# Optimization experiments

Measured on AMD Instinct MI355X. Metric: run time of the kernel, lower is better.

The kernel has to match this reference:

```python
import jax, jax.numpy as jnp
import numpy as np

M, IN, OUT = 32, 4096, 16384

def setup_inputs() -> dict:
    key = jax.random.key(0)
    k1, k2, k3 = jax.random.split(key, 3)
    x = jax.random.normal(k1, (M, IN), dtype=jnp.float32)
    weight_q = jax.random.randint(k2, (OUT, IN), 0, 256, dtype=jnp.int32)  # uint8 codes
    bias = jax.random.normal(k3, (OUT,), dtype=jnp.float32)
    return {"x": x, "weight_q": weight_q, "zero": 128, "scale": jnp.float32(0.01), "bias": bias}

def reference(x, weight_q, zero, scale, bias):
    # Dequantize: w = scale * (q - zero), per-tensor affine
    w = scale * (weight_q.astype(jnp.float32) - jnp.float32(zero))  # [OUT, IN]
    # F.linear: y = x @ w.T + b
    return jnp.einsum('mi,oi->mo', x, w) + bias
```

## Files before the change

kernel.cpp:

```cpp
#include <hip/hip_runtime.h>

#define M_DIM 32
#define K_DIM 4096
#define N_DIM 16384

using short8 = __attribute__((ext_vector_type(8))) short;
using f32x4  = __attribute__((ext_vector_type(4))) float;

__device__ __forceinline__ ushort f2bf_rne(float f) {
    unsigned u = __float_as_uint(f);
    u += 0x7fffu + ((u >> 16) & 1u);
    return (ushort)(u >> 16);
}

__device__ __forceinline__ ushort i2bf_exact(int v) {
    return (ushort)(__float_as_uint((float)v) >> 16);
}

__global__ __launch_bounds__(256) void prep_x_kernel(const float* __restrict__ x,
                                                     ushort* __restrict__ xb) {
    int i = blockIdx.x * blockDim.x + threadIdx.x;
    float4 v = reinterpret_cast<const float4*>(x)[i];
    ushort4 o;
    o.x = f2bf_rne(v.x); o.y = f2bf_rne(v.y); o.z = f2bf_rne(v.z); o.w = f2bf_rne(v.w);
    reinterpret_cast<ushort4*>(xb)[i] = o;
}

__global__ __launch_bounds__(256, 4) void qgemm_kernel(
        const ushort* __restrict__ xb, const int* __restrict__ wq,
        const int* __restrict__ zerop, const float* __restrict__ scalep,
        const float* __restrict__ bias, float* __restrict__ out) {
    const int n0   = blockIdx.x << 4;
    const int wave = threadIdx.x >> 6;
    const int lane = threadIdx.x & 63;
    const int quad = lane >> 4;
    const int l16  = lane & 15;
    const int zero = *zerop;

    const int k0 = wave << 10;

    const ushort* ap0 = xb + (size_t)l16 * K_DIM + k0 + (quad << 3);
    const ushort* ap1 = ap0 + 16 * K_DIM;
    const int* bp = wq + (size_t)(n0 + l16) * K_DIM + k0 + (quad << 3);

    f32x4 acc0 = {0.f, 0.f, 0.f, 0.f};
    f32x4 acc1 = {0.f, 0.f, 0.f, 0.f};

    #pragma unroll 4
    for (int ks = 0; ks < 32; ++ks) {
        short8 a0 = *reinterpret_cast<const short8*>(ap0);
        short8 a1 = *reinterpret_cast<const short8*>(ap1);
        int4 b0 = *reinterpret_cast<const int4*>(bp);
        int4 b1 = *reinterpret_cast<const int4*>(bp + 4);

        short8 bf;
        bf[0] = (short)i2bf_exact(b0.x - zero);
        bf[1] = (short)i2bf_exact(b0.y - zero);
        bf[2] = (short)i2bf_exact(b0.z - zero);
        bf[3] = (short)i2bf_exact(b0.w - zero);
        bf[4] = (short)i2bf_exact(b1.x - zero);
        bf[5] = (short)i2bf_exact(b1.y - zero);
        bf[6] = (short)i2bf_exact(b1.z - zero);
        bf[7] = (short)i2bf_exact(b1.w - zero);

        acc0 = __builtin_amdgcn_mfma_f32_16x16x32_bf16(a0, bf, acc0, 0, 0, 0);
        acc1 = __builtin_amdgcn_mfma_f32_16x16x32_bf16(a1, bf, acc1, 0, 0, 0);

        ap0 += 32; ap1 += 32; bp += 32;
    }

    __shared__ float red[4][32][16];
    #pragma unroll
    for (int i = 0; i < 4; ++i) {
        red[wave][(quad << 2) + i][l16]      = acc0[i];
        red[wave][16 + (quad << 2) + i][l16] = acc1[i];
    }
    __syncthreads();

    const float scale = *scalep;
    #pragma unroll
    for (int t = 0; t < 2; ++t) {
        int idx = threadIdx.x + (t << 8);
        int row = idx >> 4;
        int c   = idx & 15;
        float s = red[0][row][c] + red[1][row][c] + red[2][row][c] + red[3][row][c];
        out[(size_t)row * N_DIM + n0 + c] = fmaf(scale, s, bias[n0 + c]);
    }
}

extern "C" void kernel_launch(void* const* d_in, const int* in_sizes, int n_in,
                              void* d_out, int out_size, void* d_ws, size_t ws_size,
                              hipStream_t stream) {
    const float* x      = (const float*)d_in[0];
    const int*   wq     = (const int*)d_in[1];
    const int*   zerop  = (const int*)d_in[2];
    const float* scalep = (const float*)d_in[3];
    const float* bias   = (const float*)d_in[4];
    float*       out    = (float*)d_out;
    ushort*      xb     = (ushort*)d_ws;

    prep_x_kernel<<<(M_DIM * K_DIM / 4) / 256, 256, 0, stream>>>(x, xb);
    qgemm_kernel<<<N_DIM / 16, 256, 0, stream>>>(xb, wq, zerop, scalep, bias, out);
}
```

Measured before the change: 376.5 us.

## Stage weight tiles through LDS with coalesced loads, register prefetch and staggered K order

Weight loads now go through a shared-memory tile. Each wave reads contiguous 128-element K chunks of its rows (coalesced int4 loads), converts them to bf16 into LDS, and the MFMA operands are read back from LDS. The next chunk is prefetched into registers while the current one is consumed. Each block starts at a different K phase, which spreads accesses across memory channels. In exchange it adds two __syncthreads per stage and drops the occupancy hint from launch bounds.

```diff
diff --git a/kernel.cpp b/kernel.cpp
--- a/kernel.cpp
+++ b/kernel.cpp
@@ -3,6 +3,10 @@
 #define M_DIM 32
 #define K_DIM 4096
 #define N_DIM 16384
+#define BN 16
+#define BK 128
+#define NSTAGE 32
+#define LROW 136
 
 using short8 = __attribute__((ext_vector_type(8))) short;
 using f32x4  = __attribute__((ext_vector_type(4))) float;
@@ -17,6 +21,15 @@
     return (ushort)(__float_as_uint((float)v) >> 16);
 }
 
+__device__ __forceinline__ ushort4 cvt4(int4 v, int zero) {
+    ushort4 o;
+    o.x = i2bf_exact(v.x - zero);
+    o.y = i2bf_exact(v.y - zero);
+    o.z = i2bf_exact(v.z - zero);
+    o.w = i2bf_exact(v.w - zero);
+    return o;
+}
+
 __global__ __launch_bounds__(256) void prep_x_kernel(const float* __restrict__ x,
                                                      ushort* __restrict__ xb) {
     int i = blockIdx.x * blockDim.x + threadIdx.x;
@@ -26,50 +39,62 @@
     reinterpret_cast<ushort4*>(xb)[i] = o;
 }
 
-__global__ __launch_bounds__(256, 4) void qgemm_kernel(
+__global__ __launch_bounds__(256) void qgemm_kernel(
         const ushort* __restrict__ xb, const int* __restrict__ wq,
         const int* __restrict__ zerop, const float* __restrict__ scalep,
         const float* __restrict__ bias, float* __restrict__ out) {
-    const int n0   = blockIdx.x << 4;
-    const int wave = threadIdx.x >> 6;
-    const int lane = threadIdx.x & 63;
+    __shared__ ushort tile[BN][LROW];
+    __shared__ float  red[4][M_DIM][BN];
+
+    const int tid  = threadIdx.x;
+    const int wave = tid >> 6;
+    const int lane = tid & 63;
     const int quad = lane >> 4;
     const int l16  = lane & 15;
+    const int n0   = blockIdx.x * BN;
     const int zero = *zerop;
+    const int phase = blockIdx.x & (NSTAGE - 1);
 
-    const int k0 = wave << 10;
+    const int srow0 = wave * 4 + (lane >> 5);
+    const int srow1 = srow0 + 2;
+    const int sofs  = (lane & 31) * 4;
+    const int* gb0 = wq + (size_t)(n0 + srow0) * K_DIM + sofs;
+    const int* gb1 = wq + (size_t)(n0 + srow1) * K_DIM + sofs;
 
-    const ushort* ap0 = xb + (size_t)l16 * K_DIM + k0 + (quad << 3);
-    const ushort* ap1 = ap0 + 16 * K_DIM;
-    const int* bp = wq + (size_t)(n0 + l16) * K_DIM + k0 + (quad << 3);
+    const int bofs = wave * 32 + quad * 8;
+    const ushort* axp0 = xb + (size_t)l16 * K_DIM + bofs;
+    const ushort* axp1 = axp0 + 16 * K_DIM;
 
     f32x4 acc0 = {0.f, 0.f, 0.f, 0.f};
     f32x4 acc1 = {0.f, 0.f, 0.f, 0.f};
 
-    #pragma unroll 4
-    for (int ks = 0; ks < 32; ++ks) {
-        short8 a0 = *reinterpret_cast<const short8*>(ap0);
-        short8 a1 = *reinterpret_cast<const short8*>(ap1);
-        int4 b0 = *reinterpret_cast<const int4*>(bp);
-        int4 b1 = *reinterpret_cast<const int4*>(bp + 4);
+    int4 c0 = *(const int4*)(gb0 + phase * BK);
+    int4 c1 = *(const int4*)(gb1 + phase * BK);
 
-        short8 bf;
-        bf[0] = (short)i2bf_exact(b0.x - zero);
-        bf[1] = (short)i2bf_exact(b0.y - zero);
-        bf[2] = (short)i2bf_exact(b0.z - zero);
-        bf[3] = (short)i2bf_exact(b0.w - zero);
-        bf[4] = (short)i2bf_exact(b1.x - zero);
-        bf[5] = (short)i2bf_exact(b1.y - zero);
-        bf[6] = (short)i2bf_exact(b1.z - zero);
-        bf[7] = (short)i2bf_exact(b1.w - zero);
+    #pragma unroll 1
+    for (int s = 0; s < NSTAGE; ++s) {
+        int4 nx0, nx1;
+        if (s + 1 < NSTAGE) {
+            int sn = ((s + 1 + phase) & (NSTAGE - 1)) * BK;
+            nx0 = *(const int4*)(gb0 + sn);
+            nx1 = *(const int4*)(gb1 + sn);
+        }
+        __syncthreads();
+        *(ushort4*)&tile[srow0][sofs] = cvt4(c0, zero);
+        *(ushort4*)&tile[srow1][sofs] = cvt4(c1, zero);
+        __syncthreads();
 
+        const int k0 = ((s + phase) & (NSTAGE - 1)) * BK;
+        short8 a0 = *(const short8*)(axp0 + k0);
+        short8 a1 = *(const short8*)(axp1 + k0);
+        short8 bf = *(const short8*)&tile[l16][bofs];
         acc0 = __builtin_amdgcn_mfma_f32_16x16x32_bf16(a0, bf, acc0, 0, 0, 0);
         acc1 = __builtin_amdgcn_mfma_f32_16x16x32_bf16(a1, bf, acc1, 0, 0, 0);
 
-        ap0 += 32; ap1 += 32; bp += 32;
+        c0 = nx0; c1 = nx1;
     }
 
-    __shared__ float red[4][32][16];
+    __syncthreads();
     #pragma unroll
     for (int i = 0; i < 4; ++i) {
         red[wave][(quad << 2) + i][l16]      = acc0[i];
@@ -80,7 +105,7 @@
     const float scale = *scalep;
     #pragma unroll
     for (int t = 0; t < 2; ++t) {
-        int idx = threadIdx.x + (t << 8);
+        int idx = tid + (t << 8);
         int row = idx >> 4;
         int c   = idx & 15;
         float s = red[0][row][c] + red[1][row][c] + red[2][row][c] + red[3][row][c];
@@ -100,5 +125,5 @@
     ushort*      xb     = (ushort*)d_ws;
 
     prep_x_kernel<<<(M_DIM * K_DIM / 4) / 256, 256, 0, stream>>>(x, xb);
-    qgemm_kernel<<<N_DIM / 16, 256, 0, stream>>>(xb, wq, zerop, scalep, bias, out);
+    qgemm_kernel<<<N_DIM / BN, 256, 0, stream>>>(xb, wq, zerop, scalep, bias, out);
 }
```

New measurement: 359.9 us. 4.4% less time.
